# Kernel tuning notes

Hardware: AMD Instinct MI355X
Metric: run time of the kernel (lower is better)

The kernel has to match this reference:

```python
import jax, jax.numpy as jnp
import numpy as np

N, Q, C, T = 32, 300, 92, 32  # batch, queries, classes, targets-per-image
L_CLS, L_IOU, L_L1 = 1.0, 2.0, 5.0


def _cxcywh_to_xyxy(b):
    cx, cy, w, h = b[..., 0], b[..., 1], b[..., 2], b[..., 3]
    return jnp.stack([cx - 0.5 * w, cy - 0.5 * h, cx + 0.5 * w, cy + 0.5 * h], axis=-1)


def _generalized_box_iou(a, b):
    # a: [P,4] xyxy, b: [M,4] xyxy -> [P,M]
    area_a = (a[:, 2] - a[:, 0]) * (a[:, 3] - a[:, 1])
    area_b = (b[:, 2] - b[:, 0]) * (b[:, 3] - b[:, 1])
    lt = jnp.maximum(a[:, None, :2], b[None, :, :2])
    rb = jnp.minimum(a[:, None, 2:], b[None, :, 2:])
    wh = jnp.clip(rb - lt, 0.0)
    inter = wh[..., 0] * wh[..., 1]
    union = area_a[:, None] + area_b[None, :] - inter
    iou = inter / union
    lt_c = jnp.minimum(a[:, None, :2], b[None, :, :2])
    rb_c = jnp.maximum(a[:, None, 2:], b[None, :, 2:])
    wh_c = jnp.clip(rb_c - lt_c, 0.0)
    area_c = wh_c[..., 0] * wh_c[..., 1]
    return iou - (area_c - union) / area_c


def _cost_matrix(pred_logits, pred_boxes, tgt_labels, tgt_boxes):
    out_prob = jax.nn.softmax(pred_logits.reshape(-1, C), axis=-1)  # [N*Q, C]
    out_bbox = pred_boxes.reshape(-1, 4)                            # [N*Q, 4]
    cost_class = -out_prob[:, tgt_labels]                           # [N*Q, N*T]
    cost_bbox = jnp.sum(jnp.abs(out_bbox[:, None, :] - tgt_boxes[None, :, :]), axis=-1)
    cost_giou = -_generalized_box_iou(_cxcywh_to_xyxy(out_bbox), _cxcywh_to_xyxy(tgt_boxes))
    cost = L_L1 * cost_bbox + L_CLS * cost_class + L_IOU * cost_giou
    return cost.reshape(N, Q, N * T)


def _lsa(cost):
    # Jonker-Volgenant shortest augmenting path (e-maxx), cost: [n, m], n <= m.
    # Returns col4row: for each row, the assigned column.
    n, m = cost.shape
    INF = np.inf
    u = np.zeros(n + 1)
    v = np.zeros(m + 1)
    p = np.zeros(m + 1, dtype=np.int64)   # p[j] = row assigned to column j (1-based)
    way = np.zeros(m + 1, dtype=np.int64)
    for i in range(1, n + 1):
        p[0] = i
        j0 = 0
        minv = np.full(m + 1, INF)
        used = np.zeros(m + 1, dtype=bool)
        while True:
            used[j0] = True
            i0 = p[j0]
            free = ~used[1:]
            cur = cost[i0 - 1] - u[i0] - v[1:]
            upd = free & (cur < minv[1:])
            minv[1:][upd] = cur[upd]
            way[1:][upd] = j0
            j1 = 1 + int(np.argmin(np.where(free, minv[1:], INF)))
            delta = minv[j1]
            used_idx = np.nonzero(used)[0]
            u[p[used_idx]] += delta
            v[used_idx] -= delta
            minv[1:][free] -= delta
            j0 = j1
            if p[j0] == 0:
                break
        while j0:
            j1 = way[j0]
            p[j0] = p[j1]
            j0 = j1
    ans = np.full(n, -1, dtype=np.int64)
    js = np.nonzero(p[1:])[0]
    ans[p[1:][js] - 1] = js
    return ans


def _multiplier(cost):
    c_np = np.asarray(jax.device_get(cost))  # [N, Q, N*T]
    mult = np.zeros_like(c_np)
    for i in range(N):
        block = c_np[i, :, i * T:(i + 1) * T]  # [Q, T], sample i's own targets
        q_of_t = _lsa(block.T)                 # for each target, matched query
        # NOTE: faithfully replicates the original code's `count = 0` reset,
        # so columns are indexed locally (first T columns of the global axis).
        mult[i, q_of_t, np.arange(T)] = 1.0
    return jnp.asarray(mult)


def setup_inputs() -> dict:
    key = jax.random.key(0)
    k1, k2, k3, k4 = jax.random.split(key, 4)
    return {
        "pred_logits": jax.random.normal(k1, (N, Q, C), dtype=jnp.float32),
        "pred_boxes": jax.random.uniform(k2, (N, Q, 4), dtype=jnp.float32),
        "tgt_labels": jax.random.randint(k3, (N * T,), 0, C, dtype=jnp.int64),
        "tgt_boxes": jax.random.uniform(k4, (N * T, 4), dtype=jnp.float32),
    }


def reference(pred_logits, pred_boxes, tgt_labels, tgt_boxes):
    cost = _cost_matrix(pred_logits, pred_boxes, tgt_labels, tgt_boxes)
    mult = _multiplier(cost)
    return jnp.sum(cost * mult)
```

## Files before the change

### kernel.cpp

```cpp
#include <hip/hip_runtime.h>
#include <cfloat>
#include <cmath>

#define Nn 32
#define Qq 300
#define Cc 92
#define Tt 32
#define KCOLS 5
#define LSTRIDE 93
#define AUCTION_ROUNDS 16

__device__ inline float wave_min_bcast(float x) {
#define DPPMIN(ctrl) { int _t = __builtin_amdgcn_update_dpp( \
        __float_as_int(x), __float_as_int(x), ctrl, 0xf, 0xf, false); \
        x = fminf(x, __int_as_float(_t)); }
    DPPMIN(0x111) DPPMIN(0x112) DPPMIN(0x114) DPPMIN(0x118)
    DPPMIN(0x142) DPPMIN(0x143)
#undef DPPMIN
    return __int_as_float(__builtin_amdgcn_readlane(__float_as_int(x), 63));
}

__device__ inline int sel5i(const int a[KCOLS], int k) {
    int r = a[0];
    if (k == 1) r = a[1];
    if (k == 2) r = a[2];
    if (k == 3) r = a[3];
    if (k == 4) r = a[4];
    return r;
}

__device__ inline float readlane_f(float v, int lane) {
    return __int_as_float(__builtin_amdgcn_readlane(__float_as_int(v), lane));
}

__device__ inline void softmax_lds(const float* __restrict__ srow,
                                   float& mx, float& inv_s) {
    float m0 = -FLT_MAX, m1 = -FLT_MAX, m2 = -FLT_MAX, m3 = -FLT_MAX;
#pragma unroll
    for (int c = 0; c < Cc; c += 4) {
        m0 = fmaxf(m0, srow[c + 0]);
        m1 = fmaxf(m1, srow[c + 1]);
        m2 = fmaxf(m2, srow[c + 2]);
        m3 = fmaxf(m3, srow[c + 3]);
    }
    const float m = fmaxf(fmaxf(m0, m1), fmaxf(m2, m3));
    float s0 = 0.f, s1 = 0.f, s2 = 0.f, s3 = 0.f;
#pragma unroll
    for (int c = 0; c < Cc; c += 4) {
        s0 += __expf(srow[c + 0] - m);
        s1 += __expf(srow[c + 1] - m);
        s2 += __expf(srow[c + 2] - m);
        s3 += __expf(srow[c + 3] - m);
    }
    mx = m; inv_s = 1.f / ((s0 + s1) + (s2 + s3));
}

__device__ inline float det_cost(float cx, float cy, float w, float h,
                                 float bcx, float bcy, float bw, float bh,
                                 float cls) {
    const float ax0 = cx - 0.5f * w, ay0 = cy - 0.5f * h;
    const float ax1 = cx + 0.5f * w, ay1 = cy + 0.5f * h;
    const float areaA = (ax1 - ax0) * (ay1 - ay0);

    const float l1 = fabsf(cx - bcx) + fabsf(cy - bcy) +
                     fabsf(w - bw) + fabsf(h - bh);

    const float bx0 = bcx - 0.5f * bw, by0 = bcy - 0.5f * bh;
    const float bx1 = bcx + 0.5f * bw, by1 = bcy + 0.5f * bh;
    const float areaB = (bx1 - bx0) * (by1 - by0);

    const float ltx = fmaxf(ax0, bx0), lty = fmaxf(ay0, by0);
    const float rbx = fminf(ax1, bx1), rby = fminf(ay1, by1);
    const float iw = fmaxf(rbx - ltx, 0.f), ih = fmaxf(rby - lty, 0.f);
    const float inter = iw * ih;
    const float uni = areaA + areaB - inter;
    const float iou = inter / uni;

    const float ex0 = fminf(ax0, bx0), ey0 = fminf(ay0, by0);
    const float ex1 = fmaxf(ax1, bx1), ey1 = fmaxf(ay1, by1);
    const float areaC = fmaxf(ex1 - ex0, 0.f) * fmaxf(ey1 - ey0, 0.f);
    const float giou = iou - (areaC - uni) / areaC;

    return 5.f * l1 + cls - 2.f * giou;
}

__global__ __launch_bounds__(320) void fused_kernel(
    const float* __restrict__ logits,
    const float* __restrict__ pboxes,
    const int*   __restrict__ tlabels,
    const float* __restrict__ tboxes,
    float* __restrict__ out)
{
    const int b = blockIdx.x;
    const int tid = threadIdx.x;

    extern __shared__ float s_lg[];
    __shared__ float s_diag[Tt * Qq];
    __shared__ float s_tb[Tt * 4];
    __shared__ int   s_tl[Tt];
    __shared__ int   pairs[Tt];
    __shared__ float s_v[Qq];
    __shared__ float s_u[Tt + 1];
    __shared__ int   s_colrow[Qq];
    __shared__ unsigned long long s_bid64[Qq];
    __shared__ int   s_rj1[Tt + 1];
    __shared__ float s_rg1[Tt + 1], s_rg2[Tt + 1];
    __shared__ unsigned s_mask;

    if (tid < Tt * 4) s_tb[tid] = tboxes[b * Tt * 4 + tid];
    if (tid < Tt)     s_tl[tid] = tlabels[b * Tt + tid];
    if (tid < Qq)     { s_v[tid] = 0.f; s_colrow[tid] = 0; }
    if (tid == 0)     s_mask = 0xffffffffu;

    {
        const float4* lgb = reinterpret_cast<const float4*>(
            logits + (size_t)b * Qq * Cc);
#pragma unroll 4
        for (int g = tid; g < Qq * 23; g += 320) {
            const float4 v = lgb[g];
            const int r = g / 23, c4 = (g - r * 23) * 4;
            float* dst = &s_lg[r * LSTRIDE + c4];
            dst[0] = v.x; dst[1] = v.y; dst[2] = v.z; dst[3] = v.w;
        }
    }
    __syncthreads();

    if (tid < Qq) {
        const float* srow = &s_lg[tid * LSTRIDE];
        float mx, inv_s;
        softmax_lds(srow, mx, inv_s);
        const float4 pbv = reinterpret_cast<const float4*>(pboxes)[b * Qq + tid];
#pragma unroll 4
        for (int t = 0; t < Tt; ++t) {
            const float cls = -__expf(srow[s_tl[t]] - mx) * inv_s;
            s_diag[t * Qq + tid] =
                det_cost(pbv.x, pbv.y, pbv.z, pbv.w,
                         s_tb[t * 4 + 0], s_tb[t * 4 + 1],
                         s_tb[t * 4 + 2], s_tb[t * 4 + 3], cls);
        }
    }
    __syncthreads();

    {
        const int w = tid >> 6, ln = tid & 63;
        const bool iv4 = (ln + 256) >= Qq;
        for (int round = 0; round < AUCTION_ROUNDS; ++round) {
            const unsigned msk = s_mask;
            if (msk == 0) break;
            for (int j = tid; j < Qq; j += 320) s_bid64[j] = 0ull;
            __syncthreads();

            {
                unsigned m = msk; int n = 0;
                while (m) {
                    const int row = __ffs(m);
                    m &= m - 1;
                    if ((n % 5) == w) {
                        const float* rowp = &s_diag[(row - 1) * Qq + ln];
                        float m1 = INFINITY, m2 = INFINITY; int a1 = 0;
                        float c;
                        c = rowp[0]   - s_v[ln];
                        if (c < m1) { m2 = m1; m1 = c; a1 = ln + 1; }   else if (c < m2) m2 = c;
                        c = rowp[64]  - s_v[ln + 64];
                        if (c < m1) { m2 = m1; m1 = c; a1 = ln + 65; }  else if (c < m2) m2 = c;
                        c = rowp[128] - s_v[ln + 128];
                        if (c < m1) { m2 = m1; m1 = c; a1 = ln + 129; } else if (c < m2) m2 = c;
                        c = rowp[192] - s_v[ln + 192];
                        if (c < m1) { m2 = m1; m1 = c; a1 = ln + 193; } else if (c < m2) m2 = c;
                        c = iv4 ? INFINITY : (rowp[256] - s_v[ln + 256]);
                        if (c < m1) { m2 = m1; m1 = c; a1 = ln + 257; } else if (c < m2) m2 = c;

                        const float g1 = wave_min_bcast(m1);
                        const unsigned long long mk = __ballot(m1 == g1);
                        const int src = __ffsll((long long)mk) - 1;
                        const float cand2 = (ln == src) ? m2 : m1;
                        const float g2 = wave_min_bcast(cand2);
                        const int j1 = __builtin_amdgcn_readlane(a1, src);
                        if (ln == 0) {
                            s_rj1[row] = j1; s_rg1[row] = g1; s_rg2[row] = g2;
                            const unsigned long long pk =
                                ((unsigned long long)(__float_as_uint(g2 - g1) + 1u) << 32)
                                | (unsigned)(0xffffffffu - (unsigned)row);
                            atomicMax(&s_bid64[j1 - 1], pk);
                        }
                    }
                    ++n;
                }
            }
            __syncthreads();

            if (tid < Tt && (msk & (1u << tid))) {
                const int row = tid + 1;
                const int j1 = s_rj1[row];
                const float g1 = s_rg1[row], g2 = s_rg2[row];
                const unsigned long long mypk =
                    ((unsigned long long)(__float_as_uint(g2 - g1) + 1u) << 32)
                    | (unsigned)(0xffffffffu - (unsigned)row);
                if (s_bid64[j1 - 1] == mypk) {
                    const int old = s_colrow[j1 - 1];
                    s_colrow[j1 - 1] = row;
                    s_v[j1 - 1] -= (g2 - g1);
                    s_u[row] = g2;
                    atomicAnd(&s_mask, ~(1u << tid));
                    if (old) atomicOr(&s_mask, 1u << (old - 1));
                } else {
                    s_u[row] = g1;
                }
            }
            __syncthreads();
        }
    }

    if (tid >= 64) return;
    const int lane = tid;
    const bool inval4 = (lane + 256) >= Qq;

    float u_reg = (lane >= 1 && lane <= Tt) ? s_u[lane] : 0.f;
    float v_r[KCOLS]; int p_r[KCOLS];
#pragma unroll
    for (int k = 0; k < KCOLS; ++k) {
        const int j = lane + 64 * k;
        v_r[k] = (j < Qq) ? s_v[j] : 0.f;
        p_r[k] = (j < Qq) ? s_colrow[j] : 0;
    }

    for (unsigned rem = s_mask; rem; rem &= rem - 1) {
        const int i = __ffs(rem);

        float minv_r[KCOLS], vmask[KCOLS], am[KCOLS];
        int way_r[KCOLS];
#pragma unroll
        for (int k = 0; k < KCOLS; ++k) {
            minv_r[k] = FLT_MAX; way_r[k] = 0;
            const bool inv = (k == 4) && inval4;
            vmask[k] = inv ? -INFINITY : v_r[k];
            am[k]    = inv ?  INFINITY : 0.f;
        }
        float markg = 0.f;
        int   ent = 0;
        int   j0 = 0, i0 = i;
        float du = 0.f - readlane_f(u_reg, i);
        int   jfinal = 0;
        float Dfinal = 0.f;

        const float* rowp = &s_diag[(i0 - 1) * Qq + lane];
        float c0 = rowp[0], c1 = rowp[64], c2 = rowp[128], c3 = rowp[192],
              c4 = rowp[256];

        while (true) {
            const float cc[KCOLS] = {c0, c1, c2, c3, c4};
            float sv[KCOLS];
#pragma unroll
            for (int k = 0; k < KCOLS; ++k) {
                const float cur = (cc[k] + du) - vmask[k];
                const bool lt = cur < minv_r[k];
                way_r[k]  = lt ? j0  : way_r[k];
                minv_r[k] = lt ? cur : minv_r[k];
                sv[k] = minv_r[k] + am[k];
            }
            float val = sv[0];
            int   kb  = 0;
#pragma unroll
            for (int k = 1; k < KCOLS; ++k)
                if (sv[k] < val) { val = sv[k]; kb = k; }

            const float gmin = wave_min_bcast(val);
            const unsigned long long mask = __ballot(val == gmin);
            const int src = __ffsll((long long)mask) - 1;
            const int colid = lane + 1 + (kb << 6);
            const int pk = (sel5i(p_r, kb) << 16) | colid;
            const int got = __builtin_amdgcn_readlane(pk, src);
            const int j1   = got & 0xffff;
            const int rowm = got >> 16;

            const int k1 = (j1 - 1) >> 6;
            const bool own = (lane == ((j1 - 1) & 63));
#pragma unroll
            for (int k = 0; k < KCOLS; ++k)
                if (own && k == k1) { vmask[k] = -INFINITY; am[k] = INFINITY; }

            if (rowm == 0) { jfinal = j1; Dfinal = gmin; break; }

            i0 = rowm; j0 = j1;
            rowp = &s_diag[(i0 - 1) * Qq + lane];
            c0 = rowp[0]; c1 = rowp[64]; c2 = rowp[128]; c3 = rowp[192];
            c4 = rowp[256];
            du = gmin - readlane_f(u_reg, i0);
            markg = (lane == rowm) ? gmin : markg;
            ent   = (lane == rowm) ? 1    : ent;
        }

#pragma unroll
        for (int k = 0; k < KCOLS; ++k) {
            bool usedk = (am[k] == INFINITY);
            if (k == 4) usedk = usedk && !inval4;
            v_r[k] -= usedk ? (Dfinal - minv_r[k]) : 0.f;
        }
        u_reg += (lane == i) ? Dfinal : (ent ? (Dfinal - markg) : 0.f);

        int jj = jfinal;
        while (jj) {
            const int ow = (jj - 1) & 63, kk = (jj - 1) >> 6;
            const int jprev = __builtin_amdgcn_readlane(sel5i(way_r, kk), ow);
            int pnew;
            if (jprev == 0) pnew = i;
            else pnew = __builtin_amdgcn_readlane(sel5i(p_r, (jprev - 1) >> 6),
                                                  (jprev - 1) & 63);
            const bool own = (lane == ow);
#pragma unroll
            for (int k = 0; k < KCOLS; ++k) if (own && k == kk) p_r[k] = pnew;
            jj = jprev;
        }
    }

#pragma unroll
    for (int k = 0; k < KCOLS; ++k)
        if (p_r[k]) pairs[p_r[k] - 1] = lane + 64 * k;
    __threadfence_block();

    float part = 0.f;
    if (lane < Tt) {
        const int q = pairs[lane];
        const float* srow = &s_lg[q * LSTRIDE];
        float mx, inv_s;
        softmax_lds(srow, mx, inv_s);
        const float4 pbv = reinterpret_cast<const float4*>(pboxes)[b * Qq + q];
        const float4 tbv = reinterpret_cast<const float4*>(tboxes)[lane];
        const float cls = -__expf(srow[tlabels[lane]] - mx) * inv_s;
        part = det_cost(pbv.x, pbv.y, pbv.z, pbv.w,
                        tbv.x, tbv.y, tbv.z, tbv.w, cls);
    }
    for (int off = 32; off > 0; off >>= 1) part += __shfl_down(part, off);
    if (lane == 0) atomicAdd(out, part);
}

extern "C" void kernel_launch(void* const* d_in, const int* in_sizes, int n_in,
                              void* d_out, int out_size, void* d_ws, size_t ws_size,
                              hipStream_t stream) {
    const float* logits  = (const float*)d_in[0];
    const float* pboxes  = (const float*)d_in[1];
    const int*   tlabels = (const int*)d_in[2];
    const float* tboxes  = (const float*)d_in[3];
    float* out = (float*)d_out;

    (void)hipMemsetAsync(out, 0, sizeof(float), stream);
    const size_t lg_bytes = (size_t)Qq * LSTRIDE * sizeof(float);
    fused_kernel<<<Nn, 320, lg_bytes, stream>>>(logits, pboxes, tlabels, tboxes, out);
}
```

Measured before the change: 83.55 us.

## Split cost computation into separate wide kernel before per-image LSA kernel

Moves the softmax and per-image cost-matrix computation out of the single 32-block fused kernel into a separate kernel using 160 blocks of 64 threads. Its results go to a workspace buffer along with per-row max and inverse-sum values. The LSA kernel then copies the precomputed cost block into LDS and reuses the saved softmax stats for the final sum. This spreads the cost phase over more CUs and frees the large logits LDS buffer from the LSA kernel, at the cost of an extra launch and a global round-trip for the cost matrix.

```diff
diff --git a/kernel.cpp b/kernel.cpp
--- a/kernel.cpp
+++ b/kernel.cpp
@@ -84,20 +84,75 @@
     return 5.f * l1 + cls - 2.f * giou;
 }
 
-__global__ __launch_bounds__(320) void fused_kernel(
+__global__ __launch_bounds__(64) void cost_kernel(
     const float* __restrict__ logits,
     const float* __restrict__ pboxes,
     const int*   __restrict__ tlabels,
     const float* __restrict__ tboxes,
+    float*  __restrict__ diag,
+    float2* __restrict__ mxinv)
+{
+    const int bid = blockIdx.x;
+    const int b = bid / 5, chunk = bid - 5 * b;
+    const int tid = threadIdx.x;
+    const int q0 = chunk * 64;
+    const int nrows = (Qq - q0 < 64) ? (Qq - q0) : 64;
+
+    __shared__ float s_lg[64 * LSTRIDE];
+    __shared__ float s_tb[Tt * 4];
+    __shared__ int   s_tl[Tt];
+
+    if (tid < Tt) {
+        const float4 tb = reinterpret_cast<const float4*>(tboxes)[b * Tt + tid];
+        s_tb[tid * 4 + 0] = tb.x; s_tb[tid * 4 + 1] = tb.y;
+        s_tb[tid * 4 + 2] = tb.z; s_tb[tid * 4 + 3] = tb.w;
+        s_tl[tid] = tlabels[b * Tt + tid];
+    }
+
+    {
+        const float4* lgb = reinterpret_cast<const float4*>(
+            logits + ((size_t)b * Qq + q0) * Cc);
+#pragma unroll 4
+        for (int g = tid; g < nrows * 23; g += 64) {
+            const float4 v = lgb[g];
+            const int r = g / 23, c4 = (g - r * 23) * 4;
+            float* dst = &s_lg[r * LSTRIDE + c4];
+            dst[0] = v.x; dst[1] = v.y; dst[2] = v.z; dst[3] = v.w;
+        }
+    }
+    __syncthreads();
+
+    if (tid >= nrows) return;
+    const int q = q0 + tid;
+    const float* srow = &s_lg[tid * LSTRIDE];
+    float mx, inv_s;
+    softmax_lds(srow, mx, inv_s);
+    mxinv[b * Qq + q] = make_float2(mx, inv_s);
+
+    const float4 pbv = reinterpret_cast<const float4*>(pboxes)[b * Qq + q];
+#pragma unroll 4
+    for (int t = 0; t < Tt; ++t) {
+        const float cls = -__expf(srow[s_tl[t]] - mx) * inv_s;
+        diag[((size_t)(b * Tt + t)) * Qq + q] =
+            det_cost(pbv.x, pbv.y, pbv.z, pbv.w,
+                     s_tb[t * 4 + 0], s_tb[t * 4 + 1],
+                     s_tb[t * 4 + 2], s_tb[t * 4 + 3], cls);
+    }
+}
+
+__global__ __launch_bounds__(320) void lsa_kernel(
+    const float*  __restrict__ diag,
+    const float2* __restrict__ mxinv,
+    const float*  __restrict__ logits,
+    const float*  __restrict__ pboxes,
+    const int*    __restrict__ tlabels,
+    const float*  __restrict__ tboxes,
     float* __restrict__ out)
 {
     const int b = blockIdx.x;
     const int tid = threadIdx.x;
 
-    extern __shared__ float s_lg[];
     __shared__ float s_diag[Tt * Qq];
-    __shared__ float s_tb[Tt * 4];
-    __shared__ int   s_tl[Tt];
     __shared__ int   pairs[Tt];
     __shared__ float s_v[Qq];
     __shared__ float s_u[Tt + 1];
@@ -107,37 +162,15 @@
     __shared__ float s_rg1[Tt + 1], s_rg2[Tt + 1];
     __shared__ unsigned s_mask;
 
-    if (tid < Tt * 4) s_tb[tid] = tboxes[b * Tt * 4 + tid];
-    if (tid < Tt)     s_tl[tid] = tlabels[b * Tt + tid];
-    if (tid < Qq)     { s_v[tid] = 0.f; s_colrow[tid] = 0; }
-    if (tid == 0)     s_mask = 0xffffffffu;
+    if (tid < Qq) { s_v[tid] = 0.f; s_colrow[tid] = 0; }
+    if (tid == 0) s_mask = 0xffffffffu;
 
     {
-        const float4* lgb = reinterpret_cast<const float4*>(
-            logits + (size_t)b * Qq * Cc);
+        const float4* src = reinterpret_cast<const float4*>(
+            diag + (size_t)b * Tt * Qq);
+        float4* dst = reinterpret_cast<float4*>(s_diag);
 #pragma unroll 4
-        for (int g = tid; g < Qq * 23; g += 320) {
-            const float4 v = lgb[g];
-            const int r = g / 23, c4 = (g - r * 23) * 4;
-            float* dst = &s_lg[r * LSTRIDE + c4];
-            dst[0] = v.x; dst[1] = v.y; dst[2] = v.z; dst[3] = v.w;
-        }
-    }
-    __syncthreads();
-
-    if (tid < Qq) {
-        const float* srow = &s_lg[tid * LSTRIDE];
-        float mx, inv_s;
-        softmax_lds(srow, mx, inv_s);
-        const float4 pbv = reinterpret_cast<const float4*>(pboxes)[b * Qq + tid];
-#pragma unroll 4
-        for (int t = 0; t < Tt; ++t) {
-            const float cls = -__expf(srow[s_tl[t]] - mx) * inv_s;
-            s_diag[t * Qq + tid] =
-                det_cost(pbv.x, pbv.y, pbv.z, pbv.w,
-                         s_tb[t * 4 + 0], s_tb[t * 4 + 1],
-                         s_tb[t * 4 + 2], s_tb[t * 4 + 3], cls);
-        }
+        for (int i = tid; i < Tt * Qq / 4; i += 320) dst[i] = src[i];
     }
     __syncthreads();
 
@@ -321,12 +354,11 @@
     float part = 0.f;
     if (lane < Tt) {
         const int q = pairs[lane];
-        const float* srow = &s_lg[q * LSTRIDE];
-        float mx, inv_s;
-        softmax_lds(srow, mx, inv_s);
+        const float2 mi = mxinv[b * Qq + q];
+        const float lgv = logits[((size_t)(b * Qq + q)) * Cc + tlabels[lane]];
+        const float cls = -__expf(lgv - mi.x) * mi.y;
         const float4 pbv = reinterpret_cast<const float4*>(pboxes)[b * Qq + q];
         const float4 tbv = reinterpret_cast<const float4*>(tboxes)[lane];
-        const float cls = -__expf(srow[tlabels[lane]] - mx) * inv_s;
         part = det_cost(pbv.x, pbv.y, pbv.z, pbv.w,
                         tbv.x, tbv.y, tbv.z, tbv.w, cls);
     }
@@ -343,7 +375,12 @@
     const float* tboxes  = (const float*)d_in[3];
     float* out = (float*)d_out;
 
+    float*  diag  = (float*)d_ws;
+    float2* mxinv = (float2*)((float*)d_ws + (size_t)Nn * Tt * Qq);
+
     (void)hipMemsetAsync(out, 0, sizeof(float), stream);
-    const size_t lg_bytes = (size_t)Qq * LSTRIDE * sizeof(float);
-    fused_kernel<<<Nn, 320, lg_bytes, stream>>>(logits, pboxes, tlabels, tboxes, out);
-}
+    cost_kernel<<<Nn * 5, 64, 0, stream>>>(logits, pboxes, tlabels, tboxes,
+                                           diag, mxinv);
+    lsa_kernel<<<Nn, 320, 0, stream>>>(diag, mxinv, logits, pboxes,
+                                       tlabels, tboxes, out);
+}
```

New measurement: 85.90 us. +2.8%, slower.

## Parallelize auction bidding across thread groups per row instead of serial wave loop

Applied to the files above, without the earlier changes.

The auction phase is reorganized so that each of the 32 target rows is scanned by a group of 10 threads, each covering 30 columns. The previous scheme had each wave serially process its share of the unassigned rows using DPP reductions. Per-thread top-two partial results go to shared memory and are merged by one thread per row before the atomic bid. The round cap drops from 16 to 12. This removes serial per-row wave iteration but adds a shared-memory merge step, and fewer rounds may leave more work to the exact fallback solver.

```diff
diff --git a/kernel.cpp b/kernel.cpp
--- a/kernel.cpp
+++ b/kernel.cpp
@@ -8,7 +8,9 @@
 #define Tt 32
 #define KCOLS 5
 #define LSTRIDE 93
-#define AUCTION_ROUNDS 16
+#define GSZ 10
+#define GCOLS 30
+#define AUCTION_ROUNDS 12
 
 __device__ inline float wave_min_bcast(float x) {
 #define DPPMIN(ctrl) { int _t = __builtin_amdgcn_update_dpp( \
@@ -103,8 +105,8 @@
     __shared__ float s_u[Tt + 1];
     __shared__ int   s_colrow[Qq];
     __shared__ unsigned long long s_bid64[Qq];
-    __shared__ int   s_rj1[Tt + 1];
-    __shared__ float s_rg1[Tt + 1], s_rg2[Tt + 1];
+    __shared__ float s_pm1[320], s_pm2[320];
+    __shared__ int   s_pa[320];
     __shared__ unsigned s_mask;
 
     if (tid < Tt * 4) s_tb[tid] = tboxes[b * Tt * 4 + tid];
@@ -142,60 +144,51 @@
     __syncthreads();
 
     {
-        const int w = tid >> 6, ln = tid & 63;
-        const bool iv4 = (ln + 256) >= Qq;
+        const int grp = tid / GSZ;
+        const int g   = tid - grp * GSZ;
         for (int round = 0; round < AUCTION_ROUNDS; ++round) {
             const unsigned msk = s_mask;
             if (msk == 0) break;
             for (int j = tid; j < Qq; j += 320) s_bid64[j] = 0ull;
-            __syncthreads();
-
-            {
-                unsigned m = msk; int n = 0;
-                while (m) {
-                    const int row = __ffs(m);
-                    m &= m - 1;
-                    if ((n % 5) == w) {
-                        const float* rowp = &s_diag[(row - 1) * Qq + ln];
-                        float m1 = INFINITY, m2 = INFINITY; int a1 = 0;
-                        float c;
-                        c = rowp[0]   - s_v[ln];
-                        if (c < m1) { m2 = m1; m1 = c; a1 = ln + 1; }   else if (c < m2) m2 = c;
-                        c = rowp[64]  - s_v[ln + 64];
-                        if (c < m1) { m2 = m1; m1 = c; a1 = ln + 65; }  else if (c < m2) m2 = c;
-                        c = rowp[128] - s_v[ln + 128];
-                        if (c < m1) { m2 = m1; m1 = c; a1 = ln + 129; } else if (c < m2) m2 = c;
-                        c = rowp[192] - s_v[ln + 192];
-                        if (c < m1) { m2 = m1; m1 = c; a1 = ln + 193; } else if (c < m2) m2 = c;
-                        c = iv4 ? INFINITY : (rowp[256] - s_v[ln + 256]);
-                        if (c < m1) { m2 = m1; m1 = c; a1 = ln + 257; } else if (c < m2) m2 = c;
-
-                        const float g1 = wave_min_bcast(m1);
-                        const unsigned long long mk = __ballot(m1 == g1);
-                        const int src = __ffsll((long long)mk) - 1;
-                        const float cand2 = (ln == src) ? m2 : m1;
-                        const float g2 = wave_min_bcast(cand2);
-                        const int j1 = __builtin_amdgcn_readlane(a1, src);
-                        if (ln == 0) {
-                            s_rj1[row] = j1; s_rg1[row] = g1; s_rg2[row] = g2;
-                            const unsigned long long pk =
-                                ((unsigned long long)(__float_as_uint(g2 - g1) + 1u) << 32)
-                                | (unsigned)(0xffffffffu - (unsigned)row);
-                            atomicMax(&s_bid64[j1 - 1], pk);
-                        }
-                    }
-                    ++n;
+
+            if (msk & (1u << grp)) {
+                const float* rowp = &s_diag[grp * Qq];
+                float m1 = INFINITY, m2 = INFINITY; int a1 = 0;
+                const int c0 = g * GCOLS;
+#pragma unroll
+                for (int j = 0; j < GCOLS; ++j) {
+                    const int cidx = c0 + j;
+                    const float c = rowp[cidx] - s_v[cidx];
+                    if (c < m1) { m2 = m1; m1 = c; a1 = cidx + 1; }
+                    else if (c < m2) m2 = c;
                 }
+                s_pm1[tid] = m1; s_pm2[tid] = m2; s_pa[tid] = a1;
             }
             __syncthreads();
 
+            float g1 = 0.f, g2 = 0.f; int j1 = 0;
+            unsigned long long mypk = 0ull;
+            if (tid < Tt && (msk & (1u << tid))) {
+                float best = INFINITY, second = INFINITY, bm2 = INFINITY;
+                int ba = 0;
+                const int base = tid * GSZ;
+#pragma unroll
+                for (int q = 0; q < GSZ; ++q) {
+                    const float v = s_pm1[base + q];
+                    if (v < best) {
+                        second = best; best = v;
+                        ba = s_pa[base + q]; bm2 = s_pm2[base + q];
+                    } else if (v < second) second = v;
+                }
+                g1 = best; g2 = fminf(second, bm2); j1 = ba;
+                mypk = ((unsigned long long)(__float_as_uint(g2 - g1) + 1u) << 32)
+                       | (unsigned)(0xffffffffu - (unsigned)(tid + 1));
+                atomicMax(&s_bid64[j1 - 1], mypk);
+            }
+            __syncthreads();
+
             if (tid < Tt && (msk & (1u << tid))) {
                 const int row = tid + 1;
-                const int j1 = s_rj1[row];
-                const float g1 = s_rg1[row], g2 = s_rg2[row];
-                const unsigned long long mypk =
-                    ((unsigned long long)(__float_as_uint(g2 - g1) + 1u) << 32)
-                    | (unsigned)(0xffffffffu - (unsigned)row);
                 if (s_bid64[j1 - 1] == mypk) {
                     const int old = s_colrow[j1 - 1];
                     s_colrow[j1 - 1] = row;
```

Result: slower. 86.20 us (+3.2%).
